# Optimization experiments

Hardware: AMD Instinct MI355X
Metric: run time of the kernel (lower is better)

## Reference

```python
import jax, jax.numpy as jnp
import numpy as np

F_DIM = 128; HID = 32; C = 8 * HID; DEPTH = 5; K = 3; HEADS = 8
JK_H = (7 * C) // 2  # 896, PyG JumpingKnowledge('lstm', C, jk_depth=7)
FLEX = 512; CLASSES = 10; GATE_H = 21 * HID
BS = 512; NPG = 23; N_NODES = BS * NPG
EPS = 1e-5


def _bn(x, gamma=None, beta=None):
    # training-mode BatchNorm1d (biased variance), affine optional
    mu = x.mean(0)
    var = x.var(0)
    y = (x - mu) * jax.lax.rsqrt(var + EPS)
    return y * gamma + beta if gamma is not None else y


def _lstm(seq, w_ih, w_hh, b_ih, b_hh):
    # seq: [T, N, C] -> hidden states [T, N, H]; torch gate order i,f,g,o
    n = seq.shape[1]
    hdim = w_hh.shape[1]
    def step(carry, xt):
        h, c = carry
        z = xt @ w_ih.T + h @ w_hh.T + b_ih + b_hh
        i, f, g, o = jnp.split(z, 4, axis=-1)
        c = jax.nn.sigmoid(f) * c + jax.nn.sigmoid(i) * jnp.tanh(g)
        h = jax.nn.sigmoid(o) * jnp.tanh(c)
        return (h, c), h
    init = (jnp.zeros((n, hdim), seq.dtype), jnp.zeros((n, hdim), seq.dtype))
    _, hs = jax.lax.scan(step, init, seq)
    return hs


def _forward(x, conv1_w, conv1_b, bn1_g, bn1_b, ll1_w, ll1_b, tag_w, tag_b,
             gat_w, gat_asrc, gat_adst, gat_b,
             lw_ih_f, lw_hh_f, lb_ih_f, lb_hh_f, lw_ih_b, lw_hh_b, lb_ih_b, lb_hh_b,
             jk_w, jk_b, fff_w1, fff_b1, fff_w2, fff_b2,
             gate_w1, gate_b1, gate_w2, gate_b2,
             conv2_w, conv2_b, bn2_g, bn2_b, fc_w, fc_b,
             edge_index, batch, num_graphs):
    n, f = x.shape
    bs = num_graphs
    # --- temporal preprocessing: PE over node axis (d_model=23), Conv1d, BN ---
    xt = x.reshape(bs, NPG, f).transpose(0, 2, 1)            # [bs, F, 23]
    pos = jnp.arange(f, dtype=x.dtype)[:, None]
    div = jnp.exp(jnp.arange(0, NPG, 2, dtype=x.dtype) * (-np.log(10000.0) / NPG))
    pe = jnp.zeros((f, NPG), x.dtype)
    pe = pe.at[:, 0::2].set(jnp.sin(pos * div))
    pe = pe.at[:, 1::2].set(jnp.cos(pos * div)[:, :(NPG - 1) // 2])
    xt = (xt + pe[None]).transpose(0, 2, 1)                  # [bs, 23, F]
    xt = jax.lax.conv_general_dilated(xt, conv1_w, (1,), [(1, 1)],
            dimension_numbers=('NCH', 'OIH', 'NCH')) + conv1_b[None, :, None]
    h = _bn(xt.reshape(n, f), bn1_g, bn1_b) @ ll1_w + ll1_b  # [N, HID]
    # --- symmetric gcn_norm (no self loops) shared by all TAGConv layers ---
    src, dst = edge_index[0], edge_index[1]
    deg = jax.ops.segment_sum(jnp.ones(src.shape, h.dtype), dst, n)
    dinv = jnp.where(deg > 0, jax.lax.rsqrt(jnp.maximum(deg, 1.0)), 0.0)
    wnorm = dinv[src] * dinv[dst]                            # [E]
    # GAT uses self loops
    loop = jnp.arange(n, dtype=src.dtype)
    src_sl = jnp.concatenate([src, loop])
    dst_sl = jnp.concatenate([dst, loop])

    jk_seq = []
    for i in range(DEPTH):
        # TAGConv: concat powers of normalized adjacency, then linear
        xs = h
        feats = [h]
        for _ in range(K):
            xs = jax.ops.segment_sum(wnorm[:, None] * xs[src], dst, n)
            feats.append(xs)
        tag = jnp.concatenate(feats, axis=-1) @ tag_w[i] + tag_b[i]
        h = _bn(h + tag)                                     # SublayerConnection (BN affine=False)
        # GATConv, heads=8, concat
        g = (h @ gat_w[i]).reshape(n, HEADS, HID)
        a = jax.nn.leaky_relu((g * gat_asrc[i]).sum(-1)[src_sl]
                              + (g * gat_adst[i]).sum(-1)[dst_sl], 0.2)  # [E', heads]
        m = jax.lax.stop_gradient(jax.ops.segment_max(a, dst_sl, n))
        ea = jnp.exp(a - m[dst_sl])
        alpha = ea / jax.ops.segment_sum(ea, dst_sl, n)[dst_sl]
        out = jax.ops.segment_sum(alpha[:, :, None] * g[src_sl], dst_sl, n)
        jk_seq.append(out.reshape(n, C) + gat_b[i])

    # JumpingKnowledge 'lstm': bi-LSTM attention over the DEPTH layer outputs
    seq = jnp.stack(jk_seq, axis=0)                          # [T=5, N, C]
    hf = _lstm(seq, lw_ih_f, lw_hh_f, lb_ih_f, lb_hh_f)
    hb = _lstm(seq[::-1], lw_ih_b, lw_hh_b, lb_ih_b, lb_hh_b)[::-1]
    att = (jnp.concatenate([hf, hb], -1) @ jk_w + jk_b)[..., 0]  # [T, N]
    w_jk = jax.nn.softmax(att, axis=0)                       # softmax over layers
    xg = (seq * w_jk[:, :, None]).sum(0)                     # [N, C]
    # FinalFeedForward + residual BN (slc4)
    ff = jax.nn.elu(xg @ fff_w1 + fff_b1) @ fff_w2 + fff_b2
    xg = _bn(xg + ff)
    # GlobalAttention pooling per graph
    gate = ((xg @ gate_w1 + gate_b1) @ gate_w2 + gate_b2)[:, 0]  # [N]
    gm = jax.lax.stop_gradient(jax.ops.segment_max(gate, batch, bs))
    ge = jnp.exp(gate - gm[batch])
    gw = ge / jax.ops.segment_sum(ge, batch, bs)[batch]
    pooled = jax.ops.segment_sum(gw[:, None] * xg, batch, bs)    # [bs, C]
    # Conv1d(1->10, k=9) over channel axis, mean over out-channels, BN, classifier
    y = jax.lax.conv_general_dilated(pooled[:, None, :], conv2_w, (1,), [(4, 4)],
            dimension_numbers=('NCH', 'OIH', 'NCH')) + conv2_b[None, :, None]
    y = _bn(y.mean(axis=1), bn2_g, bn2_b)
    return jax.nn.log_softmax(y @ fc_w + fc_b, axis=1)


def setup_inputs() -> dict:
    key = jax.random.key(0)
    it = iter(jax.random.split(key, 48))
    def rn(shape, scale=0.05):
        return jax.random.normal(next(it), shape, dtype=jnp.float32) * scale
    # complete digraph (no self loops) inside each 23-node graph
    s, d = np.meshgrid(np.arange(NPG), np.arange(NPG), indexing='ij')
    mask = s != d
    s, d = s[mask], d[mask]
    off = (np.arange(BS) * NPG)[:, None]
    src = (off + s[None, :]).reshape(-1)
    dst = (off + d[None, :]).reshape(-1)
    edge_index = jnp.asarray(np.stack([src, dst]), dtype=jnp.int32)
    batch = jnp.repeat(jnp.arange(BS, dtype=jnp.int32), NPG)
    return dict(
        x=rn((N_NODES, F_DIM), 1.0),
        edge_index=edge_index, batch=batch, num_graphs=BS,
        conv1_w=rn((NPG, NPG, 3)), conv1_b=rn((NPG,)),
        bn1_g=jnp.ones((F_DIM,), jnp.float32), bn1_b=jnp.zeros((F_DIM,), jnp.float32),
        ll1_w=rn((F_DIM, HID)), ll1_b=rn((HID,)),
        tag_w=rn((DEPTH, (K + 1) * HID, HID)), tag_b=rn((DEPTH, HID)),
        gat_w=rn((DEPTH, HID, HEADS * HID)), gat_asrc=rn((DEPTH, HEADS, HID)),
        gat_adst=rn((DEPTH, HEADS, HID)), gat_b=rn((DEPTH, HEADS * HID)),
        lw_ih_f=rn((4 * JK_H, C)), lw_hh_f=rn((4 * JK_H, JK_H)),
        lb_ih_f=rn((4 * JK_H,)), lb_hh_f=rn((4 * JK_H,)),
        lw_ih_b=rn((4 * JK_H, C)), lw_hh_b=rn((4 * JK_H, JK_H)),
        lb_ih_b=rn((4 * JK_H,)), lb_hh_b=rn((4 * JK_H,)),
        jk_w=rn((2 * JK_H, 1)), jk_b=rn((1,)),
        fff_w1=rn((C, FLEX)), fff_b1=rn((FLEX,)),
        fff_w2=rn((FLEX, C)), fff_b2=rn((C,)),
        gate_w1=rn((C, GATE_H)), gate_b1=rn((GATE_H,)),
        gate_w2=rn((GATE_H, 1)), gate_b2=rn((1,)),
        conv2_w=rn((10, 1, 9)), conv2_b=rn((10,)),
        bn2_g=jnp.ones((C,), jnp.float32), bn2_b=jnp.zeros((C,), jnp.float32),
        fc_w=rn((C, CLASSES)), fc_b=rn((CLASSES,)),
    )


def reference(x, edge_index, batch, num_graphs, conv1_w, conv1_b, bn1_g, bn1_b,
              ll1_w, ll1_b, tag_w, tag_b, gat_w, gat_asrc, gat_adst, gat_b,
              lw_ih_f, lw_hh_f, lb_ih_f, lb_hh_f, lw_ih_b, lw_hh_b, lb_ih_b, lb_hh_b,
              jk_w, jk_b, fff_w1, fff_b1, fff_w2, fff_b2,
              gate_w1, gate_b1, gate_w2, gate_b2,
              conv2_w, conv2_b, bn2_g, bn2_b, fc_w, fc_b):
    return _forward(x, conv1_w, conv1_b, bn1_g, bn1_b, ll1_w, ll1_b, tag_w, tag_b,
                    gat_w, gat_asrc, gat_adst, gat_b,
                    lw_ih_f, lw_hh_f, lb_ih_f, lb_hh_f, lw_ih_b, lw_hh_b, lb_ih_b, lb_hh_b,
                    jk_w, jk_b, fff_w1, fff_b1, fff_w2, fff_b2,
                    gate_w1, gate_b1, gate_w2, gate_b2,
                    conv2_w, conv2_b, bn2_g, bn2_b, fc_w, fc_b,
                    edge_index, batch, num_graphs)
```

## Files before the change

### kernel.cpp

```cpp
#include <hip/hip_runtime.h>
#include <math.h>

#define NNODES 11776
#define NGR    512
#define NPG    23
#define FDIM   128
#define HID    32
#define CDIM   256
#define JKH    896
#define ZCOLS  3584
#define EPSBN  1e-5f

typedef long long i64;
typedef unsigned short ushort_t;
typedef __attribute__((ext_vector_type(8))) short bf16x8;
typedef __attribute__((ext_vector_type(4))) float f32x4;

__device__ __forceinline__ float sigmoidf_(float x) { return 1.f / (1.f + expf(-x)); }

__device__ __forceinline__ ushort_t f2bf(float x) {
  unsigned u = __float_as_uint(x);
  return (ushort_t)((u + 0x7fffu + ((u >> 16) & 1u)) >> 16);
}
__device__ __forceinline__ float bf2f(ushort_t b) {
  return __uint_as_float(((unsigned)b) << 16);
}

__device__ __forceinline__ void gload16(const ushort_t* g, ushort_t* l) {
  __builtin_amdgcn_global_load_lds(
      (const __attribute__((address_space(1))) void*)g,
      (__attribute__((address_space(3))) void*)l, 16, 0, 0);
}

__global__ __launch_bounds__(256) void conv1_kernel(
    const float* __restrict__ x, const float* __restrict__ w,
    const float* __restrict__ bias, float* __restrict__ out,
    float* __restrict__ stats) {
  int b = blockIdx.x;
  __shared__ float in[NPG][FDIM];
  __shared__ float wsh[NPG * NPG * 3];
  __shared__ float cs[FDIM], cq[FDIM];
  int tid = threadIdx.x;
  if (tid < FDIM) { cs[tid] = 0.f; cq[tid] = 0.f; }
  const float c0 = -2.f * logf(10000.f) / 23.f;
  for (int idx = tid; idx < NPG * FDIM; idx += 256) {
    int p = idx >> 7, f = idx & 127;
    int j = p >> 1;
    float ang = (float)f * expf(c0 * (float)j);
    float pe = (p & 1) ? cosf(ang) : sinf(ang);
    in[p][f] = x[(i64)(b * NPG + p) * FDIM + f] + pe;
  }
  for (int idx = tid; idx < NPG * NPG * 3; idx += 256) wsh[idx] = w[idx];
  __syncthreads();
  float ls = 0.f, lq = 0.f;
  int fme = tid & 127;
  for (int idx = tid; idx < NPG * FDIM; idx += 256) {
    int o = idx >> 7, f = idx & 127;
    float acc = bias[o];
    for (int i = 0; i < NPG; ++i) {
      const float* wr = &wsh[(o * NPG + i) * 3];
      float s = in[i][f] * wr[1];
      if (f > 0)   s += in[i][f - 1] * wr[0];
      if (f < 127) s += in[i][f + 1] * wr[2];
      acc += s;
    }
    out[(i64)(b * NPG + o) * FDIM + f] = acc;
    ls += acc; lq += acc * acc;
  }
  atomicAdd(&cs[fme], ls);
  atomicAdd(&cq[fme], lq);
  __syncthreads();
  if (tid < FDIM) {
    atomicAdd(&stats[tid], cs[tid]);
    atomicAdd(&stats[FDIM + tid], cq[tid]);
  }
}

__global__ __launch_bounds__(256) void col_stats(
    const float* __restrict__ X, int rows, int cols, float* __restrict__ acc) {
  int rpt = 256 / cols;
  int c = threadIdx.x % cols;
  int rsub = threadIdx.x / cols;
  float s = 0.f, q = 0.f;
  for (int r0 = blockIdx.x * rpt; r0 < rows; r0 += gridDim.x * rpt) {
    int r = r0 + rsub;
    if (r < rows) {
      float v = X[(i64)r * cols + c];
      s += v; q += v * v;
    }
  }
  __shared__ float sh[256];
  sh[threadIdx.x] = s;
  __syncthreads();
  if (threadIdx.x < cols) {
    float t = 0.f;
    for (int g = 0; g < rpt; ++g) t += sh[g * cols + c];
    atomicAdd(&acc[c], t);
  }
  __syncthreads();
  sh[threadIdx.x] = q;
  __syncthreads();
  if (threadIdx.x < cols) {
    float t = 0.f;
    for (int g = 0; g < rpt; ++g) t += sh[g * cols + c];
    atomicAdd(&acc[cols + c], t);
  }
}

__global__ void bn_norm(const float* __restrict__ X, float* __restrict__ Y,
                        const float* __restrict__ acc, int rows, int cols) {
  i64 total = (i64)rows * cols;
  i64 idx = (i64)blockIdx.x * 256 + threadIdx.x;
  i64 stride = (i64)gridDim.x * 256;
  float invR = 1.f / (float)rows;
  for (; idx < total; idx += stride) {
    int c = (int)(idx % cols);
    float mu = acc[c] * invR;
    float var = acc[cols + c] * invR - mu * mu;
    Y[idx] = (X[idx] - mu) * rsqrtf(var + EPSBN);
  }
}

__global__ __launch_bounds__(256) void fold_ll1(
    const float* __restrict__ acc, const float* __restrict__ g,
    const float* __restrict__ be, const float* __restrict__ w,
    const float* __restrict__ lb, float* __restrict__ Wp, float* __restrict__ bp) {
  int tid = threadIdx.x;
  const float invR = 1.f / (float)NNODES;
  for (int idx = tid; idx < FDIM * HID; idx += 256) {
    int k = idx >> 5;
    float mu = acc[k] * invR;
    float var = acc[FDIM + k] * invR - mu * mu;
    float scale = g[k] * rsqrtf(var + EPSBN);
    Wp[idx] = scale * w[idx];
  }
  if (tid < HID) {
    float s = lb[tid];
    for (int k = 0; k < FDIM; ++k) {
      float mu = acc[k] * invR;
      float var = acc[FDIM + k] * invR - mu * mu;
      float scale = g[k] * rsqrtf(var + EPSBN);
      s += (be[k] - mu * scale) * w[k * HID + tid];
    }
    bp[tid] = s;
  }
}

template <int BT>
__global__ __launch_bounds__(256) void sgemm(
    const float* __restrict__ A, const float* __restrict__ B, float* __restrict__ C,
    int M, int N, int K,
    const float* __restrict__ bias, const float* __restrict__ resid,
    int act, int accumulate) {
  __shared__ float As[16][128];
  __shared__ float Bs[16][128];
  int tid = threadIdx.x;
  int bm0 = blockIdx.x * 128;
  int bn0 = blockIdx.y * 128;
  int tx = tid & 15, ty = tid >> 4;
  float acc[8][8];
#pragma unroll
  for (int i = 0; i < 8; ++i)
#pragma unroll
    for (int j = 0; j < 8; ++j) acc[i][j] = 0.f;

  int ar = tid >> 2;
  int akc = (tid & 3) << 2;
  bool bfull = (bn0 + 127 < N);

  for (int k0 = 0; k0 < K; k0 += 16) {
    {
      const float* ap = A + (i64)(bm0 + ar) * K + k0 + akc;
      float4 a0 = *(const float4*)ap;
      float4 a1 = *(const float4*)(ap + (i64)64 * K);
      As[akc + 0][ar] = a0.x; As[akc + 1][ar] = a0.y;
      As[akc + 2][ar] = a0.z; As[akc + 3][ar] = a0.w;
      As[akc + 0][ar + 64] = a1.x; As[akc + 1][ar + 64] = a1.y;
      As[akc + 2][ar + 64] = a1.z; As[akc + 3][ar + 64] = a1.w;
    }
    if (BT) {
      int br = tid >> 1;
      int bkc = (tid & 1) << 3;
      const float* bp = B + (i64)(bn0 + br) * K + k0 + bkc;
      float4 b0 = *(const float4*)bp;
      float4 b1 = *(const float4*)(bp + 4);
      Bs[bkc + 0][br] = b0.x; Bs[bkc + 1][br] = b0.y;
      Bs[bkc + 2][br] = b0.z; Bs[bkc + 3][br] = b0.w;
      Bs[bkc + 4][br] = b1.x; Bs[bkc + 5][br] = b1.y;
      Bs[bkc + 6][br] = b1.z; Bs[bkc + 7][br] = b1.w;
    } else {
      int bk = tid >> 4;
      int bn = (tid & 15) << 3;
      const float* bp = B + (i64)(k0 + bk) * N + bn0 + bn;
      if (bfull) {
        *(float4*)&Bs[bk][bn] = *(const float4*)bp;
        *(float4*)&Bs[bk][bn + 4] = *(const float4*)(bp + 4);
      } else {
#pragma unroll
        for (int q = 0; q < 8; ++q)
          Bs[bk][bn + q] = (bn0 + bn + q < N) ? bp[q] : 0.f;
      }
    }
    __syncthreads();
#pragma unroll
    for (int kk = 0; kk < 16; ++kk) {
      float a[8], b[8];
      *(float4*)(a)     = *(const float4*)&As[kk][ty * 8];
      *(float4*)(a + 4) = *(const float4*)&As[kk][ty * 8 + 4];
      *(float4*)(b)     = *(const float4*)&Bs[kk][tx * 8];
      *(float4*)(b + 4) = *(const float4*)&Bs[kk][tx * 8 + 4];
#pragma unroll
      for (int i = 0; i < 8; ++i)
#pragma unroll
        for (int j = 0; j < 8; ++j)
          acc[i][j] = fmaf(a[i], b[j], acc[i][j]);
    }
    __syncthreads();
  }
#pragma unroll
  for (int i = 0; i < 8; ++i) {
    int m = bm0 + ty * 8 + i;
#pragma unroll
    for (int j = 0; j < 8; ++j) {
      int n = bn0 + tx * 8 + j;
      if (n < N) {
        i64 ci = (i64)m * N + n;
        float v = acc[i][j];
        if (accumulate) {
          C[ci] += v;
        } else {
          if (bias) v += bias[n];
          if (act == 1) v = v > 0.f ? v : expm1f(v);
          if (resid) v += resid[ci];
          C[ci] = v;
        }
      }
    }
  }
}

__global__ __launch_bounds__(256) void tag_fused(
    const float* __restrict__ hbuf, const float* __restrict__ tag_w,
    const float* __restrict__ tag_b, float* __restrict__ hres,
    float* __restrict__ stats) {
  int b = blockIdx.x, tid = threadIdx.x;
  __shared__ float fe[NPG][FDIM];
  __shared__ float wsh[FDIM * HID];
  __shared__ float S[HID];
  __shared__ float cs[HID], cq[HID];
  if (tid < HID) { cs[tid] = 0.f; cq[tid] = 0.f; }
  const float* hp = hbuf + (i64)b * NPG * HID;
  for (int idx = tid; idx < NPG * HID; idx += 256) fe[idx >> 5][idx & 31] = hp[idx];
  for (int idx = tid; idx < FDIM * HID; idx += 256) wsh[idx] = tag_w[idx];
  __syncthreads();
  if (tid < HID) {
    float s = 0.f;
    for (int p = 0; p < NPG; ++p) s += fe[p][tid];
    S[tid] = s;
  }
  __syncthreads();
  const float wn = 1.f / 22.f;
  for (int idx = tid; idx < NPG * HID; idx += 256) {
    int p = idx >> 5, c = idx & 31;
    float f0 = fe[p][c], Sc = S[c];
    float f1 = (Sc - f0) * wn;
    float f2 = (Sc - f1) * wn;
    float f3 = (Sc - f2) * wn;
    fe[p][HID + c] = f1;
    fe[p][2 * HID + c] = f2;
    fe[p][3 * HID + c] = f3;
  }
  __syncthreads();
  for (int idx = tid; idx < NPG * HID; idx += 256) {
    int p = idx >> 5, c = idx & 31;
    float acc = tag_b[c];
#pragma unroll 8
    for (int k = 0; k < FDIM; ++k) acc += fe[p][k] * wsh[k * HID + c];
    float v = fe[p][c] + acc;
    hres[(i64)(b * NPG + p) * HID + c] = v;
    atomicAdd(&cs[c], v);
    atomicAdd(&cq[c], v * v);
  }
  __syncthreads();
  if (tid < HID) {
    atomicAdd(&stats[tid], cs[tid]);
    atomicAdd(&stats[HID + tid], cq[tid]);
  }
}

__global__ __launch_bounds__(256) void gat_tag_fused(
    const float* __restrict__ hres, const float* __restrict__ stats,
    const float* __restrict__ gat_w, const float* __restrict__ asrc,
    const float* __restrict__ adst, const float* __restrict__ gbias,
    ushort_t* __restrict__ outseq,
    const float* __restrict__ tag_w_next, const float* __restrict__ tag_b_next,
    float* __restrict__ hres_out, float* __restrict__ stats_next, int has_next) {
  int b = blockIdx.x, tid = threadIdx.x;
  __shared__ float hn[NPG * HID];
  __shared__ float ssrc[NPG * 8], sdst[NPG * 8], sinv[NPG * 8];
  __shared__ float buf[10120];
  __shared__ float S[HID], cs[HID], cq[HID];
  float* gsh = buf;
  float* ealpha = buf + 5888;
  const float invR = 1.f / (float)NNODES;
  for (int idx = tid; idx < NPG * HID; idx += 256) {
    int c = idx & 31;
    float mu = stats[c] * invR;
    float var = stats[HID + c] * invR - mu * mu;
    hn[idx] = (hres[(i64)b * NPG * HID + idx] - mu) * rsqrtf(var + EPSBN);
  }
  __syncthreads();
  for (int idx = tid; idx < NPG * CDIM; idx += 256) {
    int p = idx >> 8, d = idx & 255;
    float acc = 0.f;
#pragma unroll
    for (int k = 0; k < HID; ++k) acc += hn[p * HID + k] * gat_w[k * CDIM + d];
    gsh[idx] = acc;
  }
  __syncthreads();
  if (tid < NPG * 8) {
    int p = tid >> 3, hd = tid & 7;
    float s1 = 0.f, s2 = 0.f;
    const float* gp = &gsh[p * CDIM + hd * 32];
#pragma unroll
    for (int d = 0; d < 32; ++d) {
      s1 += gp[d] * asrc[hd * 32 + d];
      s2 += gp[d] * adst[hd * 32 + d];
    }
    ssrc[tid] = s1;
    sdst[tid] = s2;
  }
  __syncthreads();
  if (tid < NPG * 8) {
    int v = tid >> 3, hd = tid & 7;
    float sd = sdst[v * 8 + hd];
    float e[NPG];
    float m = -1e30f;
#pragma unroll
    for (int u = 0; u < NPG; ++u) {
      float xv = ssrc[u * 8 + hd] + sd;
      xv = xv > 0.f ? xv : 0.2f * xv;
      e[u] = xv;
      m = fmaxf(m, xv);
    }
    float s = 0.f;
#pragma unroll
    for (int u = 0; u < NPG; ++u) {
      float t = expf(e[u] - m);
      ealpha[(v * NPG + u) * 8 + hd] = t;
      s += t;
    }
    sinv[tid] = 1.f / s;
  }
  __syncthreads();
  {
    int hd = tid >> 5, d = tid & 31;
    const i64 base = (i64)b * NPG * CDIM;
    for (int v = 0; v < NPG; ++v) {
      float acc = 0.f;
#pragma unroll
      for (int u = 0; u < NPG; ++u)
        acc += ealpha[(v * NPG + u) * 8 + hd] * gsh[u * CDIM + hd * 32 + d];
      outseq[base + (i64)v * CDIM + hd * 32 + d] =
          f2bf(acc * sinv[v * 8 + hd] + gbias[hd * 32 + d]);
    }
  }
  if (!has_next) return;
  __syncthreads();
  float* fe = buf;
  float* wsh = buf + 2944;
  if (tid < HID) { cs[tid] = 0.f; cq[tid] = 0.f; }
  for (int idx = tid; idx < FDIM * HID; idx += 256) wsh[idx] = tag_w_next[idx];
  for (int idx = tid; idx < NPG * HID; idx += 256)
    fe[(idx >> 5) * FDIM + (idx & 31)] = hn[idx];
  __syncthreads();
  if (tid < HID) {
    float s = 0.f;
    for (int p = 0; p < NPG; ++p) s += fe[p * FDIM + tid];
    S[tid] = s;
  }
  __syncthreads();
  const float wn = 1.f / 22.f;
  for (int idx = tid; idx < NPG * HID; idx += 256) {
    int p = idx >> 5, c = idx & 31;
    float f0 = fe[p * FDIM + c], Sc = S[c];
    float f1 = (Sc - f0) * wn;
    float f2 = (Sc - f1) * wn;
    float f3 = (Sc - f2) * wn;
    fe[p * FDIM + HID + c] = f1;
    fe[p * FDIM + 2 * HID + c] = f2;
    fe[p * FDIM + 3 * HID + c] = f3;
  }
  __syncthreads();
  for (int idx = tid; idx < NPG * HID; idx += 256) {
    int p = idx >> 5, c = idx & 31;
    float acc = tag_b_next[c];
#pragma unroll 8
    for (int k = 0; k < FDIM; ++k) acc += fe[p * FDIM + k] * wsh[k * HID + c];
    float v = fe[p * FDIM + c] + acc;
    hres_out[(i64)(b * NPG + p) * HID + c] = v;
    atomicAdd(&cs[c], v);
    atomicAdd(&cq[c], v * v);
  }
  __syncthreads();
  if (tid < HID) {
    atomicAdd(&stats_next[tid], cs[tid]);
    atomicAdd(&stats_next[HID + tid], cq[tid]);
  }
}

__global__ void pack_w(const float* __restrict__ w, ushort_t* __restrict__ wp,
                       int ldK) {
  i64 total = (i64)ZCOLS * ldK;
  i64 idx = (i64)blockIdx.x * 256 + threadIdx.x;
  i64 stride = (i64)gridDim.x * 256;
  for (; idx < total; idx += stride) {
    int r = (int)(idx / ldK), k = (int)(idx % ldK);
    int g = r / JKH, jj = r % JKH;
    int p = (jj >> 4) * 64 + g * 16 + (jj & 15);
    wp[(i64)p * ldK + k] = f2bf(w[idx]);
  }
}

__global__ void pack_b(const float* __restrict__ a, const float* __restrict__ b,
                       float* __restrict__ bp) {
  int r = blockIdx.x * 256 + threadIdx.x;
  if (r < ZCOLS) {
    int g = r / JKH, jj = r % JKH;
    int p = (jj >> 4) * 64 + g * 16 + (jj & 15);
    bp[p] = a[r] + b[r];
  }
}

__global__ void pack_t(const float* __restrict__ w, ushort_t* __restrict__ wt,
                       int K, int N) {
  i64 total = (i64)K * N;
  i64 idx = (i64)blockIdx.x * 256 + threadIdx.x;
  i64 stride = (i64)gridDim.x * 256;
  for (; idx < total; idx += stride) {
    int k = (int)(idx / N), n = (int)(idx % N);
    wt[(i64)n * K + k] = f2bf(w[idx]);
  }
}

template <int HASH>
__global__ __launch_bounds__(256) void lstm_step(
    const ushort_t* __restrict__ Aseq,
    const ushort_t* __restrict__ Wih,
    const ushort_t* __restrict__ Hprev,
    const ushort_t* __restrict__ Whh,
    const float*  __restrict__ bspk,
    float* __restrict__ Cst,
    ushort_t* __restrict__ Hout,
    const float* __restrict__ jkw,
    float* __restrict__ attp) {
  __shared__ ushort_t As[128 * 64];
  __shared__ ushort_t Bs[128 * 64];
  __shared__ float att_s[128];
  int tid = threadIdx.x;
  int w = tid >> 6, lane = tid & 63;
  int m0 = blockIdx.x * 128;
  int n0 = blockIdx.y * 128;
  f32x4 acc[4][4];
#pragma unroll
  for (int a = 0; a < 4; ++a)
#pragma unroll
    for (int b = 0; b < 4; ++b) acc[a][b] = (f32x4){0.f, 0.f, 0.f, 0.f};

  const ushort_t* aptr = Aseq;
  const ushort_t* bptr = Wih;
  int lda = CDIM, K = CDIM;
  for (int phase = 0; phase < (HASH ? 2 : 1); ++phase) {
    for (int k0 = 0; k0 < K; k0 += 64) {
#pragma unroll
      for (int i = 0; i < 4; ++i) {
        int r = w + i * 4;
        int s = r * 64 + lane;
        int row = s >> 3;
        int kc = (s & 7) ^ (row & 7);
        gload16(aptr + (i64)(m0 + row) * lda + k0 + kc * 8, &As[r * 512]);
        gload16(bptr + (i64)(n0 + row) * lda + k0 + kc * 8, &Bs[r * 512]);
      }
      __syncthreads();
#pragma unroll
      for (int ks = 0; ks < 2; ++ks) {
        bf16x8 af[4], bfr[4];
        int kq = ks * 4 + (lane >> 4);
#pragma unroll
        for (int mi = 0; mi < 4; ++mi) {
          int row = (w & 1) * 64 + mi * 16 + (lane & 15);
          int pos = row * 8 + (kq ^ (row & 7));
          af[mi] = *(const bf16x8*)&As[pos * 8];
        }
#pragma unroll
        for (int ni = 0; ni < 4; ++ni) {
          int row = (w >> 1) * 64 + ni * 16 + (lane & 15);
          int pos = row * 8 + (kq ^ (row & 7));
          bfr[ni] = *(const bf16x8*)&Bs[pos * 8];
        }
#pragma unroll
        for (int mi = 0; mi < 4; ++mi)
#pragma unroll
          for (int ni = 0; ni < 4; ++ni)
            acc[mi][ni] = __builtin_amdgcn_mfma_f32_16x16x32_bf16(
                af[mi], bfr[ni], acc[mi][ni], 0, 0, 0);
      }
      __syncthreads();
    }
    aptr = Hprev; bptr = Whh; lda = JKH; K = JKH;
  }

  if (tid < 128) att_s[tid] = 0.f;
  __syncthreads();

  int jb = (n0 >> 6) + (w >> 1);
  int j = jb * 16 + (lane & 15);
  float jw = jkw[j];
  float bsi = bspk[jb * 64 + (lane & 15)];
  float bsf = bspk[jb * 64 + 16 + (lane & 15)];
  float bsg = bspk[jb * 64 + 32 + (lane & 15)];
  float bso = bspk[jb * 64 + 48 + (lane & 15)];
#pragma unroll
  for (int mi = 0; mi < 4; ++mi) {
#pragma unroll
    for (int reg = 0; reg < 4; ++reg) {
      int mloc = (w & 1) * 64 + mi * 16 + (lane >> 4) * 4 + reg;
      int m = m0 + mloc;
      float zi = acc[mi][0][reg] + bsi;
      float zf = acc[mi][1][reg] + bsf;
      float zg = acc[mi][2][reg] + bsg;
      float zo = acc[mi][3][reg] + bso;
      i64 ci = (i64)m * JKH + j;
      float cv = sigmoidf_(zi) * tanhf(zg);
      if (HASH) cv += sigmoidf_(zf) * Cst[ci];
      Cst[ci] = cv;
      float hv = sigmoidf_(zo) * tanhf(cv);
      Hout[ci] = f2bf(hv);
      float av = hv * jw;
      av += __shfl_xor(av, 1, 64);
      av += __shfl_xor(av, 2, 64);
      av += __shfl_xor(av, 4, 64);
      av += __shfl_xor(av, 8, 64);
      if ((lane & 15) == 0) atomicAdd(&att_s[mloc], av);
    }
  }
  __syncthreads();
  if (tid < 128) atomicAdd(&attp[m0 + tid], att_s[tid]);
}

template <int ACT, int BF16OUT>
__global__ __launch_bounds__(256) void mfma_gemm(
    const ushort_t* __restrict__ A, const ushort_t* __restrict__ Bt, int K,
    const float* __restrict__ bias, const float* __restrict__ resid,
    float* __restrict__ Cf, ushort_t* __restrict__ Cb, int N) {
  __shared__ ushort_t As[128 * 64];
  __shared__ ushort_t Bs[128 * 64];
  int tid = threadIdx.x;
  int w = tid >> 6, lane = tid & 63;
  int m0 = blockIdx.x * 128;
  int n0 = blockIdx.y * 128;
  f32x4 acc[4][4];
#pragma unroll
  for (int a = 0; a < 4; ++a)
#pragma unroll
    for (int b = 0; b < 4; ++b) acc[a][b] = (f32x4){0.f, 0.f, 0.f, 0.f};

  for (int k0 = 0; k0 < K; k0 += 64) {
#pragma unroll
    for (int i = 0; i < 4; ++i) {
      int r = w + i * 4;
      int s = r * 64 + lane;
      int row = s >> 3;
      int kc = (s & 7) ^ (row & 7);
      gload16(A + (i64)(m0 + row) * K + k0 + kc * 8, &As[r * 512]);
      gload16(Bt + (i64)(n0 + row) * K + k0 + kc * 8, &Bs[r * 512]);
    }
    __syncthreads();
#pragma unroll
    for (int ks = 0; ks < 2; ++ks) {
      bf16x8 af[4], bfr[4];
      int kq = ks * 4 + (lane >> 4);
#pragma unroll
      for (int mi = 0; mi < 4; ++mi) {
        int row = (w & 1) * 64 + mi * 16 + (lane & 15);
        int pos = row * 8 + (kq ^ (row & 7));
        af[mi] = *(const bf16x8*)&As[pos * 8];
      }
#pragma unroll
      for (int ni = 0; ni < 4; ++ni) {
        int row = (w >> 1) * 64 + ni * 16 + (lane & 15);
        int pos = row * 8 + (kq ^ (row & 7));
        bfr[ni] = *(const bf16x8*)&Bs[pos * 8];
      }
#pragma unroll
      for (int mi = 0; mi < 4; ++mi)
#pragma unroll
        for (int ni = 0; ni < 4; ++ni)
          acc[mi][ni] = __builtin_amdgcn_mfma_f32_16x16x32_bf16(
              af[mi], bfr[ni], acc[mi][ni], 0, 0, 0);
    }
    __syncthreads();
  }
#pragma unroll
  for (int ni = 0; ni < 4; ++ni) {
    int n = n0 + (w >> 1) * 64 + ni * 16 + (lane & 15);
    float bv = bias[n];
#pragma unroll
    for (int mi = 0; mi < 4; ++mi) {
#pragma unroll
      for (int reg = 0; reg < 4; ++reg) {
        int m = m0 + (w & 1) * 64 + mi * 16 + (lane >> 4) * 4 + reg;
        float v = acc[mi][ni][reg] + bv;
        if (ACT) v = v > 0.f ? v : expm1f(v);
        i64 ci = (i64)m * N + n;
        if (BF16OUT) Cb[ci] = f2bf(v);
        else Cf[ci] = v + resid[ci];
      }
    }
  }
}

__global__ __launch_bounds__(256) void jk_combine(const float* __restrict__ att,
                                                  const ushort_t* __restrict__ seq,
                                                  float* __restrict__ xg,
                                                  ushort_t* __restrict__ xgb) {
  int n = blockIdx.x, c = threadIdx.x;
  float a[5];
  float m = -1e30f;
#pragma unroll
  for (int t = 0; t < 5; ++t) {
    a[t] = att[(i64)t * NNODES + n] + att[(i64)(5 + t) * NNODES + n];
    m = fmaxf(m, a[t]);
  }
  float s = 0.f;
#pragma unroll
  for (int t = 0; t < 5; ++t) { a[t] = expf(a[t] - m); s += a[t]; }
  float inv = 1.f / s;
  float acc = 0.f;
#pragma unroll
  for (int t = 0; t < 5; ++t)
    acc += bf2f(seq[((i64)t * NNODES + n) * CDIM + c]) * (a[t] * inv);
  xg[(i64)n * CDIM + c] = acc;
  xgb[(i64)n * CDIM + c] = f2bf(acc);
}

__global__ void fill0(float* __restrict__ p, i64 nfloat) {
  i64 i = (i64)blockIdx.x * 256 + threadIdx.x;
  i64 stride = (i64)gridDim.x * 256;
  for (; i < nfloat; i += stride) p[i] = 0.f;
}

__global__ __launch_bounds__(256) void fold_gate(
    const float* __restrict__ w1, const float* __restrict__ b1,
    const float* __restrict__ w2, const float* __restrict__ b2,
    float* __restrict__ v, float* __restrict__ b0) {
  int tid = threadIdx.x;
  float s = 0.f;
  for (int j = 0; j < 672; ++j) s += w1[tid * 672 + j] * w2[j];
  v[tid] = s;
  float p = 0.f;
  for (int j = tid; j < 672; j += 256) p += b1[j] * w2[j];
  __shared__ float sh[4];
#pragma unroll
  for (int o = 32; o > 0; o >>= 1) p += __shfl_down(p, o, 64);
  if ((tid & 63) == 0) sh[tid >> 6] = p;
  __syncthreads();
  if (tid == 0) b0[0] = sh[0] + sh[1] + sh[2] + sh[3] + b2[0];
}

__global__ __launch_bounds__(256) void pool_kernel(
    const float* __restrict__ xgn, const float* __restrict__ v,
    const float* __restrict__ b0, float* __restrict__ pooled) {
  int g = blockIdx.x, tid = threadIdx.x;
  __shared__ float gw[NPG];
  __shared__ float sh[4];
  float myv = v[tid];
  for (int p = 0; p < NPG; ++p) {
    float val = xgn[(i64)(g * NPG + p) * CDIM + tid] * myv;
#pragma unroll
    for (int o = 32; o > 0; o >>= 1) val += __shfl_down(val, o, 64);
    if ((tid & 63) == 0) sh[tid >> 6] = val;
    __syncthreads();
    if (tid == 0) gw[p] = sh[0] + sh[1] + sh[2] + sh[3] + b0[0];
    __syncthreads();
  }
  if (tid == 0) {
    float m = -1e30f;
    for (int p = 0; p < NPG; ++p) m = fmaxf(m, gw[p]);
    float s = 0.f;
    for (int p = 0; p < NPG; ++p) { gw[p] = expf(gw[p] - m); s += gw[p]; }
    float inv = 1.f / s;
    for (int p = 0; p < NPG; ++p) gw[p] *= inv;
  }
  __syncthreads();
  float acc = 0.f;
  for (int p = 0; p < NPG; ++p)
    acc += gw[p] * xgn[(i64)(g * NPG + p) * CDIM + tid];
  pooled[(i64)g * CDIM + tid] = acc;
}

__global__ void fold_conv2(const float* __restrict__ w, const float* __restrict__ b,
                           float* __restrict__ wbar) {
  int tid = threadIdx.x;
  if (tid < 9) {
    float s = 0.f;
    for (int o = 0; o < 10; ++o) s += w[o * 9 + tid];
    wbar[tid] = s * 0.1f;
  } else if (tid == 9) {
    float s = 0.f;
    for (int o = 0; o < 10; ++o) s += b[o];
    wbar[9] = s * 0.1f;
  }
}

__global__ __launch_bounds__(256) void conv2mean(const float* __restrict__ pooled,
                                                 const float* __restrict__ wbar,
                                                 float* __restrict__ y2) {
  int b = blockIdx.x, h = threadIdx.x;
  __shared__ float row[CDIM];
  row[h] = pooled[(i64)b * CDIM + h];
  __syncthreads();
  float s = wbar[9];
#pragma unroll
  for (int t = 0; t < 9; ++t) {
    int hh = h + t - 4;
    if (hh >= 0 && hh < CDIM) s += row[hh] * wbar[t];
  }
  y2[(i64)b * CDIM + h] = s;
}

__global__ __launch_bounds__(256) void final_fc(
    const float* __restrict__ y2, const float* __restrict__ acc,
    const float* __restrict__ g2, const float* __restrict__ b2,
    const float* __restrict__ fcw, const float* __restrict__ fcb,
    float* __restrict__ out) {
  int b = blockIdx.x, tid = threadIdx.x;
  __shared__ float yn[CDIM];
  __shared__ float logits[10];
  __shared__ float red[2];
  float mu = acc[tid] / 512.f;
  float var = acc[CDIM + tid] / 512.f - mu * mu;
  yn[tid] = (y2[(i64)b * CDIM + tid] - mu) * rsqrtf(var + EPSBN) * g2[tid] + b2[tid];
  __syncthreads();
  if (tid < 10) {
    float s = fcb[tid];
    for (int h = 0; h < CDIM; ++h) s += yn[h] * fcw[h * 10 + tid];
    logits[tid] = s;
  }
  __syncthreads();
  if (tid == 0) {
    float m = -1e30f;
    for (int o = 0; o < 10; ++o) m = fmaxf(m, logits[o]);
    float s = 0.f;
    for (int o = 0; o < 10; ++o) s += expf(logits[o] - m);
    red[0] = m;
    red[1] = logf(s);
  }
  __syncthreads();
  if (tid < 10) out[(i64)b * 10 + tid] = logits[tid] - red[0] - red[1];
}

extern "C" void kernel_launch(void* const* d_in, const int* in_sizes, int n_in,
                              void* d_out, int out_size, void* d_ws, size_t ws_size,
                              hipStream_t stream) {
  (void)in_sizes; (void)n_in; (void)out_size;
  const float* x        = (const float*)d_in[0];
  const float* conv1_w  = (const float*)d_in[4];
  const float* conv1_b  = (const float*)d_in[5];
  const float* bn1_g    = (const float*)d_in[6];
  const float* bn1_b    = (const float*)d_in[7];
  const float* ll1_w    = (const float*)d_in[8];
  const float* ll1_b    = (const float*)d_in[9];
  const float* tag_w    = (const float*)d_in[10];
  const float* tag_b    = (const float*)d_in[11];
  const float* gat_w    = (const float*)d_in[12];
  const float* gat_asrc = (const float*)d_in[13];
  const float* gat_adst = (const float*)d_in[14];
  const float* gat_b    = (const float*)d_in[15];
  const float* lw_ih[2] = {(const float*)d_in[16], (const float*)d_in[20]};
  const float* lw_hh[2] = {(const float*)d_in[17], (const float*)d_in[21]};
  const float* lb_ih[2] = {(const float*)d_in[18], (const float*)d_in[22]};
  const float* lb_hh[2] = {(const float*)d_in[19], (const float*)d_in[23]};
  const float* jk_w     = (const float*)d_in[24];
  const float* fff_w1   = (const float*)d_in[26];
  const float* fff_b1   = (const float*)d_in[27];
  const float* fff_w2   = (const float*)d_in[28];
  const float* fff_b2   = (const float*)d_in[29];
  const float* gate_w1  = (const float*)d_in[30];
  const float* gate_b1  = (const float*)d_in[31];
  const float* gate_w2  = (const float*)d_in[32];
  const float* gate_b2  = (const float*)d_in[33];
  const float* conv2_w  = (const float*)d_in[34];
  const float* conv2_b  = (const float*)d_in[35];
  const float* bn2_g    = (const float*)d_in[36];
  const float* bn2_b    = (const float*)d_in[37];
  const float* fc_w     = (const float*)d_in[38];
  const float* fc_b     = (const float*)d_in[39];
  float* out = (float*)d_out;

  float* ws = (float*)d_ws;
  i64 off = 0;
  auto alloc = [&](i64 n) { float* p = ws + off; off += (n + 15) & ~(i64)15; return p; };
  ushort_t* seqb = (ushort_t*)alloc(7536640);
  float* att = alloc(10 * NNODES);
  float* st1 = alloc(256);
  float* st2 = alloc(6 * 64);
  float* st4 = alloc(512);
  float* st5 = alloc(512);
  i64 zcount = (i64)(st5 - att) + 512;
  float* xg     = alloc((i64)NNODES * CDIM);
  ushort_t* xgb = (ushort_t*)alloc((i64)NNODES * CDIM / 2);
  float* hbuf   = alloc((i64)NNODES * HID);
  float* hres   = alloc((i64)NNODES * HID);
  float* Wp     = alloc(FDIM * HID);
  float* bp     = alloc(64);
  ushort_t* wihb[2]; ushort_t* whhb[2]; float* bspk[2];
  for (int d = 0; d < 2; ++d) {
    wihb[d] = (ushort_t*)alloc((i64)ZCOLS * CDIM / 2);
    whhb[d] = (ushort_t*)alloc((i64)ZCOLS * JKH / 2);
    bspk[d] = alloc(ZCOLS);
  }
  ushort_t* w1t = (ushort_t*)alloc(512 * 256 / 2);
  ushort_t* w2t = (ushort_t*)alloc(256 * 512 / 2);
  float* gatev  = alloc(CDIM);
  float* gateb0 = alloc(16);
  float* wbar   = alloc(16);
  float* pooled = alloc((i64)NGR * CDIM);
  float* y2     = alloc((i64)NGR * CDIM);
  float* Zs = ws + off;
  i64 S = (i64)(ws_size / 4) - off;
  if (S < 0) S = 0;

  int Tch = (int)(S / 172032); if (Tch < 1) Tch = 1; if (Tch > 92) Tch = 92;
  i64 Sff = S - 6029312;
  int Tf = (int)(Sff / 32768); if (Tf < 1) Tf = 1; if (Tf > 92) Tf = 92;

  float* xconv = Zs;
  ushort_t* hA = (ushort_t*)Zs;
  ushort_t* hB = hA + (i64)Tch * 128 * JKH;
  float* cch   = (float*)(hB + (i64)Tch * 128 * JKH);
  float* s4  = Zs;
  float* xgn = s4 + 3014656;
  ushort_t* ff1b = (ushort_t*)(xgn + 3014656);

  fill0<<<512, 256, 0, stream>>>(att, zcount);
  for (int d = 0; d < 2; ++d) {
    pack_w<<<2048, 256, 0, stream>>>(lw_ih[d], wihb[d], CDIM);
    pack_w<<<4096, 256, 0, stream>>>(lw_hh[d], whhb[d], JKH);
    pack_b<<<14, 256, 0, stream>>>(lb_ih[d], lb_hh[d], bspk[d]);
  }
  pack_t<<<512, 256, 0, stream>>>(fff_w1, w1t, CDIM, 512);
  pack_t<<<512, 256, 0, stream>>>(fff_w2, w2t, 512, CDIM);

  conv1_kernel<<<NGR, 256, 0, stream>>>(x, conv1_w, conv1_b, xconv, st1);
  fold_ll1<<<1, 256, 0, stream>>>(st1, bn1_g, bn1_b, ll1_w, ll1_b, Wp, bp);
  sgemm<0><<<dim3(92, 1), 256, 0, stream>>>(xconv, Wp, hbuf, NNODES, HID, FDIM,
                                            bp, nullptr, 0, 0);

  tag_fused<<<NGR, 256, 0, stream>>>(hbuf, tag_w, tag_b, hres, st2);
  for (int i = 0; i < 5; ++i) {
    int nx = (i < 4) ? (i + 1) : 0;
    gat_tag_fused<<<NGR, 256, 0, stream>>>(
        hres, st2 + i * 64, gat_w + (i64)i * HID * CDIM,
        gat_asrc + i * 256, gat_adst + i * 256, gat_b + i * 256,
        seqb + (i64)i * NNODES * CDIM,
        tag_w + (i64)nx * FDIM * HID, tag_b + nx * HID,
        hres, st2 + (i + 1) * 64, (i < 4) ? 1 : 0);
  }

  for (int dir = 0; dir < 2; ++dir) {
    for (int t0 = 0; t0 < 92; t0 += Tch) {
      int tiles = (92 - t0 < Tch) ? (92 - t0) : Tch;
      i64 r0 = (i64)t0 * 128;
      ushort_t* hp[2] = {hA, hB};
      for (int t = 0; t < 5; ++t) {
        int ts = dir ? 4 - t : t;
        const ushort_t* Ax = seqb + ((i64)ts * NNODES + r0) * CDIM;
        float* attp = att + (i64)(dir * 5 + ts) * NNODES + r0;
        if (t == 0)
          lstm_step<0><<<dim3(tiles, 28), 256, 0, stream>>>(
              Ax, wihb[dir], nullptr, nullptr, bspk[dir], cch, hp[0],
              jk_w + dir * JKH, attp);
        else
          lstm_step<1><<<dim3(tiles, 28), 256, 0, stream>>>(
              Ax, wihb[dir], hp[(t + 1) & 1], whhb[dir], bspk[dir], cch, hp[t & 1],
              jk_w + dir * JKH, attp);
      }
    }
  }
  jk_combine<<<NNODES, 256, 0, stream>>>(att, seqb, xg, xgb);

  for (int t0 = 0; t0 < 92; t0 += Tf) {
    int tiles = (92 - t0 < Tf) ? (92 - t0) : Tf;
    i64 r0 = (i64)t0 * 128;
    mfma_gemm<1, 1><<<dim3(tiles, 4), 256, 0, stream>>>(
        xgb + r0 * CDIM, w1t, CDIM, fff_b1, nullptr, nullptr, ff1b, 512);
    mfma_gemm<0, 0><<<dim3(tiles, 2), 256, 0, stream>>>(
        ff1b, w2t, 512, fff_b2, xg + r0 * CDIM, s4 + r0 * CDIM, nullptr, CDIM);
  }
  col_stats<<<184, 256, 0, stream>>>(s4, NNODES, CDIM, st4);
  bn_norm<<<4096, 256, 0, stream>>>(s4, xgn, st4, NNODES, CDIM);

  fold_gate<<<1, 256, 0, stream>>>(gate_w1, gate_b1, gate_w2, gate_b2, gatev, gateb0);
  pool_kernel<<<NGR, 256, 0, stream>>>(xgn, gatev, gateb0, pooled);
  fold_conv2<<<1, 64, 0, stream>>>(conv2_w, conv2_b, wbar);
  conv2mean<<<NGR, 256, 0, stream>>>(pooled, wbar, y2);
  col_stats<<<64, 256, 0, stream>>>(y2, NGR, CDIM, st5);
  final_fc<<<NGR, 256, 0, stream>>>(y2, st5, bn2_g, bn2_b, fc_w, fc_b, out);
}
```

Measured before the change: 1.763 ms.

## Fuse BN stats into FFN GEMM epilogue and normalize inside pool kernel

The second FFN GEMM now accumulates per-column sum and sum-of-squares in its epilogue, using shared-memory atomics and then global atomics. This removes the separate col_stats pass. The bn_norm kernel and its xgn buffer are gone: pool_kernel normalizes each graph's rows into shared memory on the fly. Separately, the LSTM gates, GAT, JK and pooling softmaxes switch to fast __expf-based sigmoid and tanh, with tanh clamped, which gives a small accuracy risk. Freeing the xgn buffer also allows larger FFN chunks.

```diff
diff --git a/kernel.cpp b/kernel.cpp
--- a/kernel.cpp
+++ b/kernel.cpp
@@ -16,7 +16,12 @@
 typedef __attribute__((ext_vector_type(8))) short bf16x8;
 typedef __attribute__((ext_vector_type(4))) float f32x4;
 
-__device__ __forceinline__ float sigmoidf_(float x) { return 1.f / (1.f + expf(-x)); }
+__device__ __forceinline__ float fsig(float x) { return 1.f / (1.f + __expf(-x)); }
+__device__ __forceinline__ float ftanh(float x) {
+  x = fminf(fmaxf(x, -15.f), 15.f);
+  float e = __expf(2.f * x);
+  return (e - 1.f) / (e + 1.f);
+}
 
 __device__ __forceinline__ ushort_t f2bf(float x) {
   unsigned u = __float_as_uint(x);
@@ -104,20 +109,6 @@
     float t = 0.f;
     for (int g = 0; g < rpt; ++g) t += sh[g * cols + c];
     atomicAdd(&acc[cols + c], t);
-  }
-}
-
-__global__ void bn_norm(const float* __restrict__ X, float* __restrict__ Y,
-                        const float* __restrict__ acc, int rows, int cols) {
-  i64 total = (i64)rows * cols;
-  i64 idx = (i64)blockIdx.x * 256 + threadIdx.x;
-  i64 stride = (i64)gridDim.x * 256;
-  float invR = 1.f / (float)rows;
-  for (; idx < total; idx += stride) {
-    int c = (int)(idx % cols);
-    float mu = acc[c] * invR;
-    float var = acc[cols + c] * invR - mu * mu;
-    Y[idx] = (X[idx] - mu) * rsqrtf(var + EPSBN);
   }
 }
 
@@ -346,7 +337,7 @@
     float s = 0.f;
 #pragma unroll
     for (int u = 0; u < NPG; ++u) {
-      float t = expf(e[u] - m);
+      float t = __expf(e[u] - m);
       ealpha[(v * NPG + u) * 8 + hd] = t;
       s += t;
     }
@@ -531,10 +522,10 @@
       float zg = acc[mi][2][reg] + bsg;
       float zo = acc[mi][3][reg] + bso;
       i64 ci = (i64)m * JKH + j;
-      float cv = sigmoidf_(zi) * tanhf(zg);
-      if (HASH) cv += sigmoidf_(zf) * Cst[ci];
+      float cv = fsig(zi) * ftanh(zg);
+      if (HASH) cv += fsig(zf) * Cst[ci];
       Cst[ci] = cv;
-      float hv = sigmoidf_(zo) * tanhf(cv);
+      float hv = fsig(zo) * ftanh(cv);
       Hout[ci] = f2bf(hv);
       float av = hv * jw;
       av += __shfl_xor(av, 1, 64);
@@ -548,13 +539,15 @@
   if (tid < 128) atomicAdd(&attp[m0 + tid], att_s[tid]);
 }
 
-template <int ACT, int BF16OUT>
+template <int ACT, int BF16OUT, int STATS>
 __global__ __launch_bounds__(256) void mfma_gemm(
     const ushort_t* __restrict__ A, const ushort_t* __restrict__ Bt, int K,
     const float* __restrict__ bias, const float* __restrict__ resid,
-    float* __restrict__ Cf, ushort_t* __restrict__ Cb, int N) {
+    float* __restrict__ Cf, ushort_t* __restrict__ Cb, int N,
+    float* __restrict__ stats) {
   __shared__ ushort_t As[128 * 64];
   __shared__ ushort_t Bs[128 * 64];
+  __shared__ float cs[128], cq[128];
   int tid = threadIdx.x;
   int w = tid >> 6, lane = tid & 63;
   int m0 = blockIdx.x * 128;
@@ -601,10 +594,16 @@
     }
     __syncthreads();
   }
+  if (STATS) {
+    if (tid < 128) { cs[tid] = 0.f; cq[tid] = 0.f; }
+    __syncthreads();
+  }
 #pragma unroll
   for (int ni = 0; ni < 4; ++ni) {
-    int n = n0 + (w >> 1) * 64 + ni * 16 + (lane & 15);
+    int nloc = (w >> 1) * 64 + ni * 16 + (lane & 15);
+    int n = n0 + nloc;
     float bv = bias[n];
+    float s = 0.f, q = 0.f;
 #pragma unroll
     for (int mi = 0; mi < 4; ++mi) {
 #pragma unroll
@@ -614,8 +613,20 @@
         if (ACT) v = v > 0.f ? v : expm1f(v);
         i64 ci = (i64)m * N + n;
         if (BF16OUT) Cb[ci] = f2bf(v);
-        else Cf[ci] = v + resid[ci];
+        else {
+          v += resid[ci];
+          Cf[ci] = v;
+          if (STATS) { s += v; q += v * v; }
+        }
       }
+    }
+    if (STATS) { atomicAdd(&cs[nloc], s); atomicAdd(&cq[nloc], q); }
+  }
+  if (STATS) {
+    __syncthreads();
+    if (tid < 128) {
+      atomicAdd(&stats[n0 + tid], cs[tid]);
+      atomicAdd(&stats[N + n0 + tid], cq[tid]);
     }
   }
 }
@@ -634,7 +645,7 @@
   }
   float s = 0.f;
 #pragma unroll
-  for (int t = 0; t < 5; ++t) { a[t] = expf(a[t] - m); s += a[t]; }
+  for (int t = 0; t < 5; ++t) { a[t] = __expf(a[t] - m); s += a[t]; }
   float inv = 1.f / s;
   float acc = 0.f;
 #pragma unroll
@@ -669,14 +680,23 @@
 }
 
 __global__ __launch_bounds__(256) void pool_kernel(
-    const float* __restrict__ xgn, const float* __restrict__ v,
-    const float* __restrict__ b0, float* __restrict__ pooled) {
+    const float* __restrict__ s4, const float* __restrict__ st,
+    const float* __restrict__ v, const float* __restrict__ b0,
+    float* __restrict__ pooled) {
   int g = blockIdx.x, tid = threadIdx.x;
+  __shared__ float xn[NPG][CDIM];
   __shared__ float gw[NPG];
   __shared__ float sh[4];
+  const float invR = 1.f / (float)NNODES;
+  float mu = st[tid] * invR;
+  float var = st[CDIM + tid] * invR - mu * mu;
+  float rs = rsqrtf(var + EPSBN);
+  for (int p = 0; p < NPG; ++p)
+    xn[p][tid] = (s4[(i64)(g * NPG + p) * CDIM + tid] - mu) * rs;
+  __syncthreads();
   float myv = v[tid];
   for (int p = 0; p < NPG; ++p) {
-    float val = xgn[(i64)(g * NPG + p) * CDIM + tid] * myv;
+    float val = xn[p][tid] * myv;
 #pragma unroll
     for (int o = 32; o > 0; o >>= 1) val += __shfl_down(val, o, 64);
     if ((tid & 63) == 0) sh[tid >> 6] = val;
@@ -688,14 +708,13 @@
     float m = -1e30f;
     for (int p = 0; p < NPG; ++p) m = fmaxf(m, gw[p]);
     float s = 0.f;
-    for (int p = 0; p < NPG; ++p) { gw[p] = expf(gw[p] - m); s += gw[p]; }
+    for (int p = 0; p < NPG; ++p) { gw[p] = __expf(gw[p] - m); s += gw[p]; }
     float inv = 1.f / s;
     for (int p = 0; p < NPG; ++p) gw[p] *= inv;
   }
   __syncthreads();
   float acc = 0.f;
-  for (int p = 0; p < NPG; ++p)
-    acc += gw[p] * xgn[(i64)(g * NPG + p) * CDIM + tid];
+  for (int p = 0; p < NPG; ++p) acc += gw[p] * xn[p][tid];
   pooled[(i64)g * CDIM + tid] = acc;
 }
 
@@ -832,7 +851,7 @@
   if (S < 0) S = 0;
 
   int Tch = (int)(S / 172032); if (Tch < 1) Tch = 1; if (Tch > 92) Tch = 92;
-  i64 Sff = S - 6029312;
+  i64 Sff = S - 3014656;
   int Tf = (int)(Sff / 32768); if (Tf < 1) Tf = 1; if (Tf > 92) Tf = 92;
 
   float* xconv = Zs;
@@ -840,8 +859,7 @@
   ushort_t* hB = hA + (i64)Tch * 128 * JKH;
   float* cch   = (float*)(hB + (i64)Tch * 128 * JKH);
   float* s4  = Zs;
-  float* xgn = s4 + 3014656;
-  ushort_t* ff1b = (ushort_t*)(xgn + 3014656);
+  ushort_t* ff1b = (ushort_t*)(s4 + 3014656);
 
   fill0<<<512, 256, 0, stream>>>(att, zcount);
   for (int d = 0; d < 2; ++d) {
@@ -893,16 +911,14 @@
   for (int t0 = 0; t0 < 92; t0 += Tf) {
     int tiles = (92 - t0 < Tf) ? (92 - t0) : Tf;
     i64 r0 = (i64)t0 * 128;
-    mfma_gemm<1, 1><<<dim3(tiles, 4), 256, 0, stream>>>(
-        xgb + r0 * CDIM, w1t, CDIM, fff_b1, nullptr, nullptr, ff1b, 512);
-    mfma_gemm<0, 0><<<dim3(tiles, 2), 256, 0, stream>>>(
-        ff1b, w2t, 512, fff_b2, xg + r0 * CDIM, s4 + r0 * CDIM, nullptr, CDIM);
-  }
-  col_stats<<<184, 256, 0, stream>>>(s4, NNODES, CDIM, st4);
-  bn_norm<<<4096, 256, 0, stream>>>(s4, xgn, st4, NNODES, CDIM);
+    mfma_gemm<1, 1, 0><<<dim3(tiles, 4), 256, 0, stream>>>(
+        xgb + r0 * CDIM, w1t, CDIM, fff_b1, nullptr, nullptr, ff1b, 512, nullptr);
+    mfma_gemm<0, 0, 1><<<dim3(tiles, 2), 256, 0, stream>>>(
+        ff1b, w2t, 512, fff_b2, xg + r0 * CDIM, s4 + r0 * CDIM, nullptr, CDIM, st4);
+  }
 
   fold_gate<<<1, 256, 0, stream>>>(gate_w1, gate_b1, gate_w2, gate_b2, gatev, gateb0);
-  pool_kernel<<<NGR, 256, 0, stream>>>(xgn, gatev, gateb0, pooled);
+  pool_kernel<<<NGR, 256, 0, stream>>>(s4, st4, gatev, gateb0, pooled);
   fold_conv2<<<1, 64, 0, stream>>>(conv2_w, conv2_b, wbar);
   conv2mean<<<NGR, 256, 0, stream>>>(pooled, wbar, y2);
   col_stats<<<64, 256, 0, stream>>>(y2, NGR, CDIM, st5);
```

Measured after the change: 1.674 ms. -5.0%, faster.
